# Kernel optimization log

Measured on AMD Instinct MI355X. Metric: run time of the kernel, lower is better.

## Reference

```python
import jax, jax.numpy as jnp
import numpy as np

T, B, C = 2048, 8, 1024
H = 8
MIN_L, MIN_R = 1, 1


def setup_inputs() -> dict:
    key = jax.random.key(0)
    k1, k2 = jax.random.split(key)
    x = jax.random.normal(k1, (T, B, C), dtype=jnp.float32)
    W_off = jax.random.normal(k2, (C, 2 * H), dtype=jnp.float32) * 0.02
    b_off = jnp.zeros((2 * H,), dtype=jnp.float32)
    return {"x": x, "W_off": W_off, "b_off": b_off}


def _interp(S, f):
    # S: (T, BH, R) cumsum; f: (T, BH) fractional index in [-1, T-1].
    # Linear interpolation of cumsum, with S(-1) == 0.
    i0 = jnp.floor(f).astype(jnp.int32)
    frac = (f - i0.astype(f.dtype))[:, :, None]
    i0c = jnp.clip(i0, 0, S.shape[0] - 1)[:, :, None]
    i1c = jnp.clip(i0 + 1, 0, S.shape[0] - 1)[:, :, None]
    v0 = jnp.where((i0 >= 0)[:, :, None], jnp.take_along_axis(S, i0c, axis=0), 0.0)
    v1 = jnp.take_along_axis(S, i1c, axis=0)
    return v0 + frac * (v1 - v0)


def reference(x, W_off, b_off):
    Tn, Bn, Cn = x.shape
    R = Cn // H
    K = MIN_L + MIN_R + 1
    # normalized cumulative sums, one lane per (batch, head)
    S = jnp.cumsum(x.reshape(Tn, Bn * H, R) * (1.0 / K), axis=0)  # (T, BH, R)
    off = jax.nn.sigmoid(x @ W_off + b_off)  # (T, B, 2H)
    aL = off[:, :, :H].reshape(Tn, Bn * H)
    aR = off[:, :, H:].reshape(Tn, Bn * H)
    t = jnp.arange(Tn, dtype=x.dtype)[:, None]  # (T, 1)
    # adaptive span lengths: minimum span plus learned fraction of max span
    lenL = MIN_L + aL * jnp.maximum(t - MIN_L, 0.0)
    lenR = MIN_R + aR * jnp.maximum((Tn - 1.0 - t) - MIN_R, 0.0)
    fL = jnp.maximum(t - lenL - 1.0, -1.0)   # left boundary - 1 (fractional)
    fR = jnp.minimum(t + lenR, Tn - 1.0)     # right boundary (fractional)
    out = _interp(S, fR) - _interp(S, fL)    # (T, BH, R)
    return out.reshape(Tn, Bn, Cn)
```

## Files before the change

### kernel.cpp

```cpp
#include <hip/hip_runtime.h>
#include <cmath>

#define T_DIM 2048
#define B_DIM 8
#define C_DIM 1024
#define H_DIM 8
#define R_DIM 128
#define BH_DIM 64
#define COLS 8192
#define COL4 2048
#define NCH 64
#define LT 32
__device__ __constant__ float INV_K = 0.33333333333333333f;

typedef _Float16 h4 __attribute__((ext_vector_type(4)));
typedef _Float16 h8 __attribute__((ext_vector_type(8)));

__global__ __launch_bounds__(256) void offsets_kernel(
        const float* __restrict__ x, const float* __restrict__ W,
        const float* __restrict__ bias, float* __restrict__ off) {
    __shared__ float Wt[16 * 1024];
    for (int idx = threadIdx.x; idx < 4096; idx += 256) {
        int c = idx >> 2, j4 = (idx & 3) * 4;
        float4 w = *reinterpret_cast<const float4*>(W + c * 16 + j4);
        Wt[(j4 + 0) * 1024 + c] = w.x;
        Wt[(j4 + 1) * 1024 + c] = w.y;
        Wt[(j4 + 2) * 1024 + c] = w.z;
        Wt[(j4 + 3) * 1024 + c] = w.w;
    }
    __syncthreads();

    int wave = threadIdx.x >> 6, lane = threadIdx.x & 63;
    int rowBase = blockIdx.x * 16 + wave * 4;
    const float* xr = x + (size_t)rowBase * C_DIM;

    float v[64];
#pragma unroll
    for (int i = 0; i < 64; ++i) v[i] = 0.f;

#pragma unroll
    for (int k = 0; k < 4; ++k) {
        int c = lane * 4 + k * 256;
        float4 xa = *reinterpret_cast<const float4*>(xr + c);
        float4 xb = *reinterpret_cast<const float4*>(xr + 1024 + c);
        float4 xc = *reinterpret_cast<const float4*>(xr + 2048 + c);
        float4 xd = *reinterpret_cast<const float4*>(xr + 3072 + c);
#pragma unroll
        for (int j = 0; j < 16; ++j) {
            float4 w = *reinterpret_cast<const float4*>(&Wt[j * 1024 + c]);
            v[j]      = fmaf(xa.x, w.x, fmaf(xa.y, w.y, fmaf(xa.z, w.z, fmaf(xa.w, w.w, v[j]))));
            v[16 + j] = fmaf(xb.x, w.x, fmaf(xb.y, w.y, fmaf(xb.z, w.z, fmaf(xb.w, w.w, v[16 + j]))));
            v[32 + j] = fmaf(xc.x, w.x, fmaf(xc.y, w.y, fmaf(xc.z, w.z, fmaf(xc.w, w.w, v[32 + j]))));
            v[48 + j] = fmaf(xd.x, w.x, fmaf(xd.y, w.y, fmaf(xd.z, w.z, fmaf(xd.w, w.w, v[48 + j]))));
        }
    }

#pragma unroll
    for (int m = 32; m >= 1; m >>= 1) {
        bool hi = (lane & m) != 0;
#pragma unroll
        for (int i = 0; i < m; ++i) {
            float send = hi ? v[i] : v[i + m];
            float recv = __shfl_xor(send, m, 64);
            v[i] = (hi ? v[i + m] : v[i]) + recv;
        }
    }

    float t = v[0] + bias[lane & 15];
    off[(size_t)rowBase * 16 + lane] = 1.f / (1.f + expf(-t));
}

__global__ void chunksum_kernel(const float4* __restrict__ x4, float4* __restrict__ csum4) {
    int gid = blockIdx.x * 256 + threadIdx.x;
    int chunk = gid >> 11;
    int col4 = gid & (COL4 - 1);
    const float4* xp = x4 + (size_t)chunk * LT * COL4 + col4;
    float sx = 0.f, sy = 0.f, sz = 0.f, sw = 0.f;
#pragma unroll 4
    for (int t = 0; t < LT; ++t) {
        float4 v = xp[(size_t)t * COL4];
        sx += v.x; sy += v.y; sz += v.z; sw += v.w;
    }
    float4 r; r.x = sx * INV_K; r.y = sy * INV_K; r.z = sz * INV_K; r.w = sw * INV_K;
    csum4[gid] = r;
}

__global__ void scan_kernel(const float4* __restrict__ x4, const float4* __restrict__ csum4,
                            _Float16* __restrict__ S) {
    int gid = blockIdx.x * 256 + threadIdx.x;
    int chunk = gid >> 11;
    int col4 = gid & (COL4 - 1);
    float rx = 0.f, ry = 0.f, rz = 0.f, rw = 0.f;
    for (int c = 0; c < chunk; ++c) {
        float4 v = csum4[c * COL4 + col4];
        rx += v.x; ry += v.y; rz += v.z; rw += v.w;
    }
    const float4* xp = x4 + (size_t)chunk * LT * COL4 + col4;
    _Float16* Sp = S + (size_t)chunk * LT * COLS + col4 * 4;
#pragma unroll 4
    for (int t = 0; t < LT; ++t) {
        float4 v = xp[(size_t)t * COL4];
        rx = fmaf(v.x, INV_K, rx);
        ry = fmaf(v.y, INV_K, ry);
        rz = fmaf(v.z, INV_K, rz);
        rw = fmaf(v.w, INV_K, rw);
        h4 o; o.x = (_Float16)rx; o.y = (_Float16)ry; o.z = (_Float16)rz; o.w = (_Float16)rw;
        *reinterpret_cast<h4*>(Sp + (size_t)t * COLS) = o;
    }
}

__global__ void gather_kernel(const _Float16* __restrict__ S, const float* __restrict__ off,
                              float* __restrict__ out) {
    int vid = blockIdx.x * 256 + threadIdx.x;
    int r8 = (vid & 15) << 3;
    int bh = (vid >> 4) & 63;
    int t = vid >> 10;
    int b = bh >> 3, h = bh & 7;
    const float* o = off + ((size_t)t * B_DIM + b) * 16;
    float aL = o[h], aR = o[8 + h];
    float tf = (float)t;
    float lenL = 1.f + aL * fmaxf(tf - 1.f, 0.f);
    float lenR = 1.f + aR * fmaxf((float)(T_DIM - 1) - tf - 1.f, 0.f);
    float fL = fmaxf(tf - lenL - 1.f, -1.f);
    float fR = fminf(tf + lenR, (float)(T_DIM - 1));
    int col = (bh << 7) | r8;

    float ffL = floorf(fL); int i0L = (int)ffL; float frL = fL - ffL;
    float ffR = floorf(fR); int i0R = (int)ffR; float frR = fR - ffR;
    int i0Lc = min(max(i0L, 0), T_DIM - 1), i1Lc = min(i0L + 1, T_DIM - 1);
    int i0Rc = min(max(i0R, 0), T_DIM - 1), i1Rc = min(i0R + 1, T_DIM - 1);

    const h8 zero8 = {0, 0, 0, 0, 0, 0, 0, 0};
    h8 v1L = *reinterpret_cast<const h8*>(S + (size_t)i1Lc * COLS + col);
    h8 v0L = (i0L >= 0) ? *reinterpret_cast<const h8*>(S + (size_t)i0Lc * COLS + col) : zero8;
    h8 v1R = *reinterpret_cast<const h8*>(S + (size_t)i1Rc * COLS + col);
    h8 v0R = (i0R >= 0) ? *reinterpret_cast<const h8*>(S + (size_t)i0Rc * COLS + col) : zero8;

    float res[8];
#pragma unroll
    for (int i = 0; i < 8; ++i) {
        float a0 = (float)v0R[i], a1 = (float)v1R[i];
        float b0 = (float)v0L[i], b1 = (float)v1L[i];
        res[i] = fmaf(frR, a1 - a0, a0) - fmaf(frL, b1 - b0, b0);
    }
    float* op = out + (size_t)vid * 8;
    *reinterpret_cast<float4*>(op)     = make_float4(res[0], res[1], res[2], res[3]);
    *reinterpret_cast<float4*>(op + 4) = make_float4(res[4], res[5], res[6], res[7]);
}

extern "C" void kernel_launch(void* const* d_in, const int* in_sizes, int n_in,
                              void* d_out, int out_size, void* d_ws, size_t ws_size,
                              hipStream_t stream) {
    const float* x = (const float*)d_in[0];
    const float* W = (const float*)d_in[1];
    const float* b = (const float*)d_in[2];

    char* ws = (char*)d_ws;
    const size_t S_bytes   = (size_t)T_DIM * COLS * sizeof(_Float16);
    const size_t off_bytes = (size_t)T_DIM * B_DIM * 16 * sizeof(float);
    _Float16* S = (_Float16*)ws;
    float* off  = (float*)(ws + S_bytes);
    float* csum = (float*)(ws + S_bytes + off_bytes);

    offsets_kernel<<<(T_DIM * B_DIM) / 16, 256, 0, stream>>>(x, W, b, off);
    chunksum_kernel<<<(NCH * COL4) / 256, 256, 0, stream>>>(
        (const float4*)x, (float4*)csum);
    scan_kernel<<<(NCH * COL4) / 256, 256, 0, stream>>>(
        (const float4*)x, (const float4*)csum, S);
    gather_kernel<<<(T_DIM * B_DIM * C_DIM / 8) / 256, 256, 0, stream>>>(
        S, off, (float*)d_out);
}
```

Measured before the change: 82.85 us.

## Fuse offset projection with chunk sums and swizzle gather block order

Merges the offset matmul and per-chunk column sums into one kernel, so x is read once for both instead of twice. Each block now owns one batch column group and one time chunk, reduces partial dot products across waves through shared memory, and writes sigmoid offsets and chunk sums together. The gather kernel also remaps block indices so that consecutive blocks are spread across time, which may improve cache locality on S. The fused kernel launches only 512 blocks and holds large per-thread accumulators, which may limit occupancy.

```diff
diff --git a/kernel.cpp b/kernel.cpp
--- a/kernel.cpp
+++ b/kernel.cpp
@@ -16,11 +16,20 @@
 typedef _Float16 h4 __attribute__((ext_vector_type(4)));
 typedef _Float16 h8 __attribute__((ext_vector_type(8)));
 
-__global__ __launch_bounds__(256) void offsets_kernel(
-        const float* __restrict__ x, const float* __restrict__ W,
-        const float* __restrict__ bias, float* __restrict__ off) {
+__global__ __launch_bounds__(256, 2) void offcsum_kernel(
+        const float4* __restrict__ x4, const float* __restrict__ W,
+        const float* __restrict__ bias, float* __restrict__ off,
+        float4* __restrict__ csum4) {
     __shared__ float Wt[16 * 1024];
-    for (int idx = threadIdx.x; idx < 4096; idx += 256) {
+    __shared__ float sdata[4][8][64];
+    const int bid = blockIdx.x;
+    const int cg = bid >> 6;
+    const int ch = bid & 63;
+    const int tid = threadIdx.x;
+    const int wave = tid >> 6, lane = tid & 63;
+    const int col4 = cg * 256 + tid;
+
+    for (int idx = tid; idx < 4096; idx += 256) {
         int c = idx >> 2, j4 = (idx & 3) * 4;
         float4 w = *reinterpret_cast<const float4*>(W + c * 16 + j4);
         Wt[(j4 + 0) * 1024 + c] = w.x;
@@ -30,59 +39,58 @@
     }
     __syncthreads();
 
-    int wave = threadIdx.x >> 6, lane = threadIdx.x & 63;
-    int rowBase = blockIdx.x * 16 + wave * 4;
-    const float* xr = x + (size_t)rowBase * C_DIM;
+    const float4* xp = x4 + (size_t)(ch * LT) * COL4 + col4;
+    const int cbase = tid * 4;
+    float csx = 0.f, csy = 0.f, csz = 0.f, csw = 0.f;
 
-    float v[64];
+#pragma unroll 1
+    for (int g = 0; g < 8; ++g) {
+        float4 xv0 = xp[(size_t)(g * 4 + 0) * COL4];
+        float4 xv1 = xp[(size_t)(g * 4 + 1) * COL4];
+        float4 xv2 = xp[(size_t)(g * 4 + 2) * COL4];
+        float4 xv3 = xp[(size_t)(g * 4 + 3) * COL4];
+        float acc[64];
 #pragma unroll
-    for (int i = 0; i < 64; ++i) v[i] = 0.f;
-
-#pragma unroll
-    for (int k = 0; k < 4; ++k) {
-        int c = lane * 4 + k * 256;
-        float4 xa = *reinterpret_cast<const float4*>(xr + c);
-        float4 xb = *reinterpret_cast<const float4*>(xr + 1024 + c);
-        float4 xc = *reinterpret_cast<const float4*>(xr + 2048 + c);
-        float4 xd = *reinterpret_cast<const float4*>(xr + 3072 + c);
+        for (int i = 0; i < 64; ++i) acc[i] = 0.f;
 #pragma unroll
         for (int j = 0; j < 16; ++j) {
-            float4 w = *reinterpret_cast<const float4*>(&Wt[j * 1024 + c]);
-            v[j]      = fmaf(xa.x, w.x, fmaf(xa.y, w.y, fmaf(xa.z, w.z, fmaf(xa.w, w.w, v[j]))));
-            v[16 + j] = fmaf(xb.x, w.x, fmaf(xb.y, w.y, fmaf(xb.z, w.z, fmaf(xb.w, w.w, v[16 + j]))));
-            v[32 + j] = fmaf(xc.x, w.x, fmaf(xc.y, w.y, fmaf(xc.z, w.z, fmaf(xc.w, w.w, v[32 + j]))));
-            v[48 + j] = fmaf(xd.x, w.x, fmaf(xd.y, w.y, fmaf(xd.z, w.z, fmaf(xd.w, w.w, v[48 + j]))));
+            float4 w = *reinterpret_cast<const float4*>(&Wt[j * 1024 + cbase]);
+            acc[j]      = fmaf(xv0.x, w.x, fmaf(xv0.y, w.y, fmaf(xv0.z, w.z, fmaf(xv0.w, w.w, acc[j]))));
+            acc[16 + j] = fmaf(xv1.x, w.x, fmaf(xv1.y, w.y, fmaf(xv1.z, w.z, fmaf(xv1.w, w.w, acc[16 + j]))));
+            acc[32 + j] = fmaf(xv2.x, w.x, fmaf(xv2.y, w.y, fmaf(xv2.z, w.z, fmaf(xv2.w, w.w, acc[32 + j]))));
+            acc[48 + j] = fmaf(xv3.x, w.x, fmaf(xv3.y, w.y, fmaf(xv3.z, w.z, fmaf(xv3.w, w.w, acc[48 + j]))));
         }
+        csx += xv0.x + xv1.x + xv2.x + xv3.x;
+        csy += xv0.y + xv1.y + xv2.y + xv3.y;
+        csz += xv0.z + xv1.z + xv2.z + xv3.z;
+        csw += xv0.w + xv1.w + xv2.w + xv3.w;
+#pragma unroll
+        for (int m = 32; m >= 1; m >>= 1) {
+            bool hi = (lane & m) != 0;
+#pragma unroll
+            for (int i = 0; i < m; ++i) {
+                float send = hi ? acc[i] : acc[i + m];
+                float recv = __shfl_xor(send, m, 64);
+                acc[i] = (hi ? acc[i + m] : acc[i]) + recv;
+            }
+        }
+        sdata[wave][g][lane] = acc[0];
     }
 
+    float4 agg; agg.x = csx * INV_K; agg.y = csy * INV_K; agg.z = csz * INV_K; agg.w = csw * INV_K;
+    csum4[(size_t)ch * COL4 + col4] = agg;
+
+    __syncthreads();
 #pragma unroll
-    for (int m = 32; m >= 1; m >>= 1) {
-        bool hi = (lane & m) != 0;
-#pragma unroll
-        for (int i = 0; i < m; ++i) {
-            float send = hi ? v[i] : v[i + m];
-            float recv = __shfl_xor(send, m, 64);
-            v[i] = (hi ? v[i + m] : v[i]) + recv;
-        }
+    for (int i = 0; i < 2; ++i) {
+        int idx = tid + i * 256;
+        int g = idx >> 6, l = idx & 63;
+        int tl = l >> 4, j = l & 15;
+        float s = sdata[0][g][l] + sdata[1][g][l] + sdata[2][g][l] + sdata[3][g][l];
+        s += bias[j];
+        int t = ch * LT + g * 4 + tl;
+        off[((size_t)t * B_DIM + cg) * 16 + j] = 1.f / (1.f + expf(-s));
     }
-
-    float t = v[0] + bias[lane & 15];
-    off[(size_t)rowBase * 16 + lane] = 1.f / (1.f + expf(-t));
-}
-
-__global__ void chunksum_kernel(const float4* __restrict__ x4, float4* __restrict__ csum4) {
-    int gid = blockIdx.x * 256 + threadIdx.x;
-    int chunk = gid >> 11;
-    int col4 = gid & (COL4 - 1);
-    const float4* xp = x4 + (size_t)chunk * LT * COL4 + col4;
-    float sx = 0.f, sy = 0.f, sz = 0.f, sw = 0.f;
-#pragma unroll 4
-    for (int t = 0; t < LT; ++t) {
-        float4 v = xp[(size_t)t * COL4];
-        sx += v.x; sy += v.y; sz += v.z; sw += v.w;
-    }
-    float4 r; r.x = sx * INV_K; r.y = sy * INV_K; r.z = sz * INV_K; r.w = sw * INV_K;
-    csum4[gid] = r;
 }
 
 __global__ void scan_kernel(const float4* __restrict__ x4, const float4* __restrict__ csum4,
@@ -111,7 +119,9 @@
 
 __global__ void gather_kernel(const _Float16* __restrict__ S, const float* __restrict__ off,
                               float* __restrict__ out) {
-    int vid = blockIdx.x * 256 + threadIdx.x;
+    int bid = blockIdx.x;
+    int sbid = (bid & 7) * 1024 + (bid >> 3);
+    int vid = sbid * 256 + threadIdx.x;
     int r8 = (vid & 15) << 3;
     int bh = (vid >> 4) & 63;
     int t = vid >> 10;
@@ -151,9 +161,9 @@
 extern "C" void kernel_launch(void* const* d_in, const int* in_sizes, int n_in,
                               void* d_out, int out_size, void* d_ws, size_t ws_size,
                               hipStream_t stream) {
-    const float* x = (const float*)d_in[0];
-    const float* W = (const float*)d_in[1];
-    const float* b = (const float*)d_in[2];
+    const float4* x4 = (const float4*)d_in[0];
+    const float* W  = (const float*)d_in[1];
+    const float* bi = (const float*)d_in[2];
 
     char* ws = (char*)d_ws;
     const size_t S_bytes   = (size_t)T_DIM * COLS * sizeof(_Float16);
@@ -162,11 +172,9 @@
     float* off  = (float*)(ws + S_bytes);
     float* csum = (float*)(ws + S_bytes + off_bytes);
 
-    offsets_kernel<<<(T_DIM * B_DIM) / 16, 256, 0, stream>>>(x, W, b, off);
-    chunksum_kernel<<<(NCH * COL4) / 256, 256, 0, stream>>>(
-        (const float4*)x, (float4*)csum);
+    offcsum_kernel<<<512, 256, 0, stream>>>(x4, W, bi, off, (float4*)csum);
     scan_kernel<<<(NCH * COL4) / 256, 256, 0, stream>>>(
-        (const float4*)x, (const float4*)csum, S);
+        x4, (const float4*)csum, S);
     gather_kernel<<<(T_DIM * B_DIM * C_DIM / 8) / 256, 256, 0, stream>>>(
         S, off, (float*)d_out);
 }
```

Measured after the change: 77.78 us. 1.07x faster.
